# Kernel tuning notes

Measured on AMD Instinct MI355X. Metric: run time of the kernel, lower is better.

Reference implementation:

```python
import jax, jax.numpy as jnp
import numpy as np

N = 2_000_000   # points
B = 4           # batch
C = 32          # feature channels
H = 512         # image height (== round(K[0,0]))
W = 512         # image width
GRID = 64       # grid_resolution


def setup_inputs() -> dict:
    key = jax.random.key(0)
    k1, k2, k3 = jax.random.split(key, 3)
    bids = jax.random.randint(k1, (N, 1), 0, B)
    coords = jax.random.randint(k2, (N, 3), 0, GRID)
    dense_coords = jnp.concatenate([bids, coords], axis=1).astype(jnp.int32)  # [N,4]
    pixel_features = jax.random.normal(k3, (B, C, H, W), dtype=jnp.float32)
    K = jnp.array([[512.0, 0.0, 256.0],
                   [0.0, 512.0, 256.0],
                   [0.0, 0.0, 1.0]], dtype=jnp.float32)
    P = jnp.array([[1.0, 0.0, 0.0, 0.0],
                   [0.0, 1.0, 0.0, 0.0],
                   [0.0, 0.0, 1.0, 3.0],
                   [0.0, 0.0, 0.0, 1.0]], dtype=jnp.float32)
    return {"dense_coords": dense_coords, "pixel_features": pixel_features, "K": K, "P": P}


def reference(dense_coords, pixel_features, K, P):
    grid_res = GRID
    batch_ids = dense_coords[:, 0]
    grid_pos = dense_coords[:, 1:].astype(pixel_features.dtype)
    # grid coords -> world positions in [-1, 1]
    world = grid_pos * (2.0 / (grid_res - 1)) - 1.0  # [N,3]
    ones = jnp.ones((world.shape[0], 1), world.dtype)
    pts_h = jnp.concatenate([world, ones], axis=1)   # [N,4]
    # project: camera = P @ pts^T, normalize by homogeneous coord
    cam = pts_h @ P.T                                # [N,4]
    cam = cam / cam[:, 3:4]
    img_h = cam[:, :3] @ K.T                         # [N,3]
    img_h = img_h / img_h[:, 2:3]
    image_x = img_h[:, 0]   # js (columns)
    image_y = img_h[:, 1]   # is (rows)
    points_depth = cam[:, 2:3]                       # [N,1]

    i0f = jnp.floor(image_y)
    j0f = jnp.floor(image_x)
    di = (image_y - i0f)[:, None]                    # [N,1]
    dj = (image_x - j0f)[:, None]                    # [N,1]

    Hh = pixel_features.shape[2]
    Ww = pixel_features.shape[3]
    i0 = jnp.clip(i0f.astype(jnp.int32), 0, Hh - 1)
    i1 = jnp.clip(i0f.astype(jnp.int32) + 1, 0, Hh - 1)
    j0 = jnp.clip(j0f.astype(jnp.int32), 0, Ww - 1)
    j1 = jnp.clip(j0f.astype(jnp.int32) + 1, 0, Ww - 1)

    b = batch_ids
    # four gathers, each [N, C] (advanced indices split by ':' -> result dims first)
    f00 = pixel_features[b, :, i0, j0]
    f10 = pixel_features[b, :, i1, j0]
    f01 = pixel_features[b, :, i0, j1]
    f11 = pixel_features[b, :, i1, j1]

    mean_j = (1.0 - di) * f00 + di * f10
    mean_jp = (1.0 - di) * f01 + di * f11
    feature_bilinear = (1.0 - dj) * mean_j + dj * mean_jp  # [N,C]
    return feature_bilinear, points_depth
```

## Files before the change

### kernel.cpp

```cpp
#include <hip/hip_runtime.h>

#define GRID_RES 64
#define C_CH     32
#define H_IMG    512
#define W_IMG    512

typedef float    f32x4 __attribute__((ext_vector_type(4)));
typedef int      i32x4 __attribute__((ext_vector_type(4)));
typedef unsigned u32x4 __attribute__((ext_vector_type(4)));

__device__ __forceinline__ ushort f32_to_bf16(float f) {
    union { float f; unsigned u; } a; a.f = f;
    unsigned r = (a.u + 0x7FFFu + ((a.u >> 16) & 1u)) >> 16;
    return (ushort)r;
}
__device__ __forceinline__ float bf16lo_to_f32(unsigned u) {
    union { unsigned u; float f; } a; a.u = u << 16; return a.f;
}
__device__ __forceinline__ float bf16hi_to_f32(unsigned u) {
    union { unsigned u; float f; } a; a.u = u & 0xFFFF0000u; return a.f;
}

__global__ __launch_bounds__(256) void transpose_bf16_kernel(
    const float* __restrict__ in, ushort* __restrict__ out)
{
    const int HW = H_IMG * W_IMG;
    __shared__ float tile[C_CH * 65];

    const int tilesPerBatch = HW / 64;
    const int b   = blockIdx.x / tilesPerBatch;
    const int t   = blockIdx.x % tilesPerBatch;
    const int hw0 = t * 64;
    const int tid = threadIdx.x;

    const int c_r = tid >> 3;
    const int u_r = (tid & 7) * 8;
    const f32x4* src = (const f32x4*)(in + ((size_t)(b * C_CH + c_r) * HW + hw0 + u_r));
    f32x4 v0 = __builtin_nontemporal_load(src);
    f32x4 v1 = __builtin_nontemporal_load(src + 1);
    float* d = &tile[c_r * 65 + u_r];
    d[0] = v0.x; d[1] = v0.y; d[2] = v0.z; d[3] = v0.w;
    d[4] = v1.x; d[5] = v1.y; d[6] = v1.z; d[7] = v1.w;

    __syncthreads();

    const int u_w = tid >> 2;
    const int c0  = (tid & 3) * 8;
    union { ushort us[8]; uint4 v; } pk;
#pragma unroll
    for (int k = 0; k < 8; ++k)
        pk.us[k] = f32_to_bf16(tile[(c0 + k) * 65 + u_w]);
    *(uint4*)(out + ((size_t)(b * HW + hw0 + u_w) * C_CH + c0)) = pk.v;
}

__global__ __launch_bounds__(256) void gather_bf16_kernel(
    const int*    __restrict__ coords,
    const ushort* __restrict__ feat,
    const float*  __restrict__ Km,
    const float*  __restrict__ Pm,
    float* __restrict__ out_feat,
    float* __restrict__ out_depth,
    int N)
{
    __shared__ int   s_base[256];
    __shared__ int   s_dji[256];
    __shared__ int   s_dii[256];
    __shared__ float s_fdi[256];
    __shared__ float s_fdj[256];

    const int tid = threadIdx.x;
    const int p0  = blockIdx.x * 256;

    {
        const int p = p0 + tid;
        if (p < N) {
            i32x4 cc = __builtin_nontemporal_load((const i32x4*)coords + p);
            const float s = 2.0f / (float)(GRID_RES - 1);
            float wx = (float)cc.y * s - 1.0f;
            float wy = (float)cc.z * s - 1.0f;
            float wz = (float)cc.w * s - 1.0f;

            float cam0 = Pm[0]  * wx + Pm[1]  * wy + Pm[2]  * wz + Pm[3];
            float cam1 = Pm[4]  * wx + Pm[5]  * wy + Pm[6]  * wz + Pm[7];
            float cam2 = Pm[8]  * wx + Pm[9]  * wy + Pm[10] * wz + Pm[11];
            float cam3 = Pm[12] * wx + Pm[13] * wy + Pm[14] * wz + Pm[15];
            cam0 /= cam3; cam1 /= cam3; cam2 /= cam3;

            float g0 = Km[0] * cam0 + Km[1] * cam1 + Km[2] * cam2;
            float g1 = Km[3] * cam0 + Km[4] * cam1 + Km[5] * cam2;
            float g2 = Km[6] * cam0 + Km[7] * cam1 + Km[8] * cam2;
            float image_x = g0 / g2;
            float image_y = g1 / g2;

            float i0f = floorf(image_y);
            float j0f = floorf(image_x);
            float di = image_y - i0f;
            float dj = image_x - j0f;
            i0f = fminf(fmaxf(i0f, -1.0e9f), 1.0e9f);
            j0f = fminf(fmaxf(j0f, -1.0e9f), 1.0e9f);
            int i0r = (int)i0f;
            int j0r = (int)j0f;
            int i0 = min(max(i0r,     0), H_IMG - 1);
            int i1 = min(max(i0r + 1, 0), H_IMG - 1);
            int j0 = min(max(j0r,     0), W_IMG - 1);
            int j1 = min(max(j0r + 1, 0), W_IMG - 1);
            int b  = cc.x;

            s_base[tid] = ((b * H_IMG + i0) * W_IMG + j0) * C_CH;
            s_dji[tid]  = (j1 - j0) * C_CH;
            s_dii[tid]  = (i1 - i0) * W_IMG * C_CH;
            s_fdi[tid]  = di;
            s_fdj[tid]  = dj;
            __builtin_nontemporal_store(cam2, out_depth + p);
        }
    }
    __syncthreads();

    const int cq   = tid & 3;
    const int slot = tid >> 2;
#pragma unroll
    for (int it = 0; it < 4; ++it) {
        const int lp = it * 64 + slot;
        const int p  = p0 + lp;
        if (p < N) {
            const int   base = s_base[lp] + cq * 8;
            const int   dji  = s_dji[lp];
            const int   dii  = s_dii[lp];
            const float fdi  = s_fdi[lp];
            const float fdj  = s_fdj[lp];

            const u32x4 u00 = *(const u32x4*)(feat + base);
            const u32x4 u01 = *(const u32x4*)(feat + base + dji);
            const u32x4 u10 = *(const u32x4*)(feat + base + dii);
            const u32x4 u11 = *(const u32x4*)(feat + base + dii + dji);

            float o[8];
            const unsigned* a00 = (const unsigned*)&u00;
            const unsigned* a01 = (const unsigned*)&u01;
            const unsigned* a10 = (const unsigned*)&u10;
            const unsigned* a11 = (const unsigned*)&u11;
#pragma unroll
            for (int k = 0; k < 4; ++k) {
                float f00 = bf16lo_to_f32(a00[k]), f01 = bf16lo_to_f32(a01[k]);
                float f10 = bf16lo_to_f32(a10[k]), f11 = bf16lo_to_f32(a11[k]);
                float r0 = f00 + fdi * (f10 - f00);
                float r1 = f01 + fdi * (f11 - f01);
                o[2 * k] = r0 + fdj * (r1 - r0);
                f00 = bf16hi_to_f32(a00[k]); f01 = bf16hi_to_f32(a01[k]);
                f10 = bf16hi_to_f32(a10[k]); f11 = bf16hi_to_f32(a11[k]);
                r0 = f00 + fdi * (f10 - f00);
                r1 = f01 + fdi * (f11 - f01);
                o[2 * k + 1] = r0 + fdj * (r1 - r0);
            }
            float* op = out_feat + (size_t)p * C_CH + cq * 8;
            f32x4 lo4 = { o[0], o[1], o[2], o[3] };
            f32x4 hi4 = { o[4], o[5], o[6], o[7] };
            __builtin_nontemporal_store(lo4, (f32x4*)op);
            __builtin_nontemporal_store(hi4, (f32x4*)(op + 4));
        }
    }
}

__global__ __launch_bounds__(256) void gather_fp32_direct_kernel(
    const int*   __restrict__ coords,
    const float* __restrict__ feat,
    const float* __restrict__ Km,
    const float* __restrict__ Pm,
    float* __restrict__ out_feat,
    float* __restrict__ out_depth,
    int N)
{
    __shared__ int   s_base[64];
    __shared__ int   s_dji[64];
    __shared__ int   s_dii[64];
    __shared__ float s_fdi[64];
    __shared__ float s_fdj[64];

    const int tid = threadIdx.x;
    const int p0  = blockIdx.x * 64;
    const int HW  = H_IMG * W_IMG;

    if (tid < 64) {
        const int p = p0 + tid;
        if (p < N) {
            int4 cc = ((const int4*)coords)[p];
            const float s = 2.0f / (float)(GRID_RES - 1);
            float wx = (float)cc.y * s - 1.0f;
            float wy = (float)cc.z * s - 1.0f;
            float wz = (float)cc.w * s - 1.0f;
            float cam0 = Pm[0]  * wx + Pm[1]  * wy + Pm[2]  * wz + Pm[3];
            float cam1 = Pm[4]  * wx + Pm[5]  * wy + Pm[6]  * wz + Pm[7];
            float cam2 = Pm[8]  * wx + Pm[9]  * wy + Pm[10] * wz + Pm[11];
            float cam3 = Pm[12] * wx + Pm[13] * wy + Pm[14] * wz + Pm[15];
            cam0 /= cam3; cam1 /= cam3; cam2 /= cam3;
            float g0 = Km[0] * cam0 + Km[1] * cam1 + Km[2] * cam2;
            float g1 = Km[3] * cam0 + Km[4] * cam1 + Km[5] * cam2;
            float g2 = Km[6] * cam0 + Km[7] * cam1 + Km[8] * cam2;
            float image_x = g0 / g2;
            float image_y = g1 / g2;
            float i0f = floorf(image_y);
            float j0f = floorf(image_x);
            float di = image_y - i0f;
            float dj = image_x - j0f;
            i0f = fminf(fmaxf(i0f, -1.0e9f), 1.0e9f);
            j0f = fminf(fmaxf(j0f, -1.0e9f), 1.0e9f);
            int i0r = (int)i0f;
            int j0r = (int)j0f;
            int i0 = min(max(i0r,     0), H_IMG - 1);
            int i1 = min(max(i0r + 1, 0), H_IMG - 1);
            int j0 = min(max(j0r,     0), W_IMG - 1);
            int j1 = min(max(j0r + 1, 0), W_IMG - 1);
            int b  = cc.x;
            s_base[tid] = (b * C_CH * H_IMG + i0) * W_IMG + j0;
            s_dji[tid]  = (j1 - j0);
            s_dii[tid]  = (i1 - i0) * W_IMG;
            s_fdi[tid]  = di;
            s_fdj[tid]  = dj;
            out_depth[p] = cam2;
        }
    }
    __syncthreads();

    const int c      = tid & 31;
    const int lpBase = tid >> 5;
#pragma unroll
    for (int it = 0; it < 8; ++it) {
        const int lp = it * 8 + lpBase;
        const int p  = p0 + lp;
        if (p < N) {
            const int   base = s_base[lp];
            const int   dji  = s_dji[lp];
            const int   dii  = s_dii[lp];
            const float fdi  = s_fdi[lp];
            const float fdj  = s_fdj[lp];
            const float* fp = feat + base + (size_t)c * HW;
            float f00 = fp[0];
            float f01 = fp[dji];
            float f10 = fp[dii];
            float f11 = fp[dii + dji];
            float r0 = f00 + fdi * (f10 - f00);
            float r1 = f01 + fdi * (f11 - f01);
            out_feat[(size_t)p * C_CH + c] = r0 + fdj * (r1 - r0);
        }
    }
}

extern "C" void kernel_launch(void* const* d_in, const int* in_sizes, int n_in,
                              void* d_out, int out_size, void* d_ws, size_t ws_size,
                              hipStream_t stream)
{
    const int*   coords = (const int*)  d_in[0];
    const float* feat   = (const float*)d_in[1];
    const float* Km     = (const float*)d_in[2];
    const float* Pm     = (const float*)d_in[3];

    const int N  = in_sizes[0] / 4;
    const int Bb = in_sizes[1] / (C_CH * H_IMG * W_IMG);
    const int HW = H_IMG * W_IMG;

    float* out_feat  = (float*)d_out;
    float* out_depth = out_feat + (size_t)N * C_CH;

    const size_t need = (size_t)in_sizes[1] * sizeof(ushort);

    if (ws_size >= need) {
        ushort* tfeat = (ushort*)d_ws;
        transpose_bf16_kernel<<<Bb * (HW / 64), 256, 0, stream>>>(feat, tfeat);
        const int nblocks = (N + 255) / 256;
        gather_bf16_kernel<<<nblocks, 256, 0, stream>>>(
            coords, tfeat, Km, Pm, out_feat, out_depth, N);
    } else {
        const int nblocks = (N + 63) / 64;
        gather_fp32_direct_kernel<<<nblocks, 64, 0, stream>>>(
            coords, feat, Km, Pm, out_feat, out_depth, N);
    }
}
```

Baseline: 474.7 us.

## Bin points by image tile via counting sort before bf16 bilinear gather

```diff
diff --git a/kernel.cpp b/kernel.cpp
--- a/kernel.cpp
+++ b/kernel.cpp
@@ -4,6 +4,7 @@
 #define C_CH     32
 #define H_IMG    512
 #define W_IMG    512
+#define NBINS    512
 
 typedef float    f32x4 __attribute__((ext_vector_type(4)));
 typedef int      i32x4 __attribute__((ext_vector_type(4)));
@@ -19,6 +20,58 @@
 }
 __device__ __forceinline__ float bf16hi_to_f32(unsigned u) {
     union { unsigned u; float f; } a; a.u = u & 0xFFFF0000u; return a.f;
+}
+
+struct ProjOut {
+    int   base;
+    int   dji;
+    int   dii;
+    float di, dj, depth;
+    int   bin;
+};
+__device__ __forceinline__ ProjOut project_pt(
+    const i32x4 cc, const float* __restrict__ Km, const float* __restrict__ Pm)
+{
+    const float s = 2.0f / (float)(GRID_RES - 1);
+    float wx = (float)cc.y * s - 1.0f;
+    float wy = (float)cc.z * s - 1.0f;
+    float wz = (float)cc.w * s - 1.0f;
+
+    float cam0 = Pm[0]  * wx + Pm[1]  * wy + Pm[2]  * wz + Pm[3];
+    float cam1 = Pm[4]  * wx + Pm[5]  * wy + Pm[6]  * wz + Pm[7];
+    float cam2 = Pm[8]  * wx + Pm[9]  * wy + Pm[10] * wz + Pm[11];
+    float cam3 = Pm[12] * wx + Pm[13] * wy + Pm[14] * wz + Pm[15];
+    cam0 /= cam3; cam1 /= cam3; cam2 /= cam3;
+
+    float g0 = Km[0] * cam0 + Km[1] * cam1 + Km[2] * cam2;
+    float g1 = Km[3] * cam0 + Km[4] * cam1 + Km[5] * cam2;
+    float g2 = Km[6] * cam0 + Km[7] * cam1 + Km[8] * cam2;
+    float image_x = g0 / g2;
+    float image_y = g1 / g2;
+
+    float i0f = floorf(image_y);
+    float j0f = floorf(image_x);
+    float di = image_y - i0f;
+    float dj = image_x - j0f;
+    i0f = fminf(fmaxf(i0f, -1.0e9f), 1.0e9f);
+    j0f = fminf(fmaxf(j0f, -1.0e9f), 1.0e9f);
+    int i0r = (int)i0f;
+    int j0r = (int)j0f;
+    int i0 = min(max(i0r,     0), H_IMG - 1);
+    int i1 = min(max(i0r + 1, 0), H_IMG - 1);
+    int j0 = min(max(j0r,     0), W_IMG - 1);
+    int j1 = min(max(j0r + 1, 0), W_IMG - 1);
+    int b  = cc.x;
+
+    ProjOut o;
+    o.base  = ((b * H_IMG + i0) * W_IMG + j0) * C_CH;
+    o.dji   = (j1 - j0) * C_CH;
+    o.dii   = (i1 - i0) * W_IMG * C_CH;
+    o.di    = di;
+    o.dj    = dj;
+    o.depth = cam2;
+    o.bin   = b * 128 + (i0 >> 5) * 8 + (j0 >> 6);
+    return o;
 }
 
 __global__ __launch_bounds__(256) void transpose_bf16_kernel(
@@ -53,6 +106,180 @@
     *(uint4*)(out + ((size_t)(b * HW + hw0 + u_w) * C_CH + c0)) = pk.v;
 }
 
+__global__ __launch_bounds__(512) void init_hist_kernel(int* __restrict__ hist)
+{
+    hist[threadIdx.x] = 0;
+}
+
+__global__ __launch_bounds__(256) void hist_kernel(
+    const int* __restrict__ coords,
+    const float* __restrict__ Km, const float* __restrict__ Pm,
+    int* __restrict__ hist, int N)
+{
+    __shared__ int lh[NBINS];
+    const int tid = threadIdx.x;
+    for (int i = tid; i < NBINS; i += 256) lh[i] = 0;
+    __syncthreads();
+
+    for (int p = blockIdx.x * 256 + tid; p < N; p += gridDim.x * 256) {
+        i32x4 cc = __builtin_nontemporal_load((const i32x4*)coords + p);
+        ProjOut o = project_pt(cc, Km, Pm);
+        atomicAdd(&lh[o.bin], 1);
+    }
+    __syncthreads();
+    for (int i = tid; i < NBINS; i += 256)
+        if (lh[i]) atomicAdd(&hist[i], lh[i]);
+}
+
+__global__ __launch_bounds__(512) void scan_kernel(
+    const int* __restrict__ hist, int* __restrict__ cursor)
+{
+    __shared__ int tmp[NBINS];
+    const int t = threadIdx.x;
+    const int v = hist[t];
+    tmp[t] = v;
+    __syncthreads();
+    for (int off = 1; off < NBINS; off <<= 1) {
+        int a = (t >= off) ? tmp[t - off] : 0;
+        __syncthreads();
+        tmp[t] += a;
+        __syncthreads();
+    }
+    cursor[t] = tmp[t] - v;
+}
+
+__global__ __launch_bounds__(1024) void scatter_kernel(
+    const int* __restrict__ coords,
+    const float* __restrict__ Km, const float* __restrict__ Pm,
+    int* __restrict__ cursor,
+    i32x4* __restrict__ records,
+    float* __restrict__ out_depth, int N)
+{
+    __shared__ int lh[NBINS];
+    __shared__ int lbase[NBINS];
+    const int tid = threadIdx.x;
+    const int p0  = blockIdx.x * 4096;
+
+    for (int i = tid; i < NBINS; i += 1024) lh[i] = 0;
+    __syncthreads();
+
+    int      binA[4], rankA[4], baseA[4];
+    unsigned pfA[4];
+    float    diA[4], djA[4];
+#pragma unroll
+    for (int k = 0; k < 4; ++k) {
+        const int pp = p0 + k * 1024 + tid;
+        binA[k] = -1;
+        if (pp < N) {
+            i32x4 cc = __builtin_nontemporal_load((const i32x4*)coords + pp);
+            ProjOut o = project_pt(cc, Km, Pm);
+            binA[k]  = o.bin;
+            baseA[k] = o.base;
+            diA[k]   = o.di;
+            djA[k]   = o.dj;
+            pfA[k]   = (unsigned)pp
+                     | ((unsigned)(o.dji != 0) << 30)
+                     | ((unsigned)(o.dii != 0) << 31);
+            rankA[k] = atomicAdd(&lh[o.bin], 1);
+            __builtin_nontemporal_store(o.depth, out_depth + pp);
+        }
+    }
+    __syncthreads();
+
+    for (int i = tid; i < NBINS; i += 1024) {
+        int c = lh[i];
+        if (c) lbase[i] = atomicAdd(&cursor[i], c);
+    }
+    __syncthreads();
+
+#pragma unroll
+    for (int k = 0; k < 4; ++k) {
+        if (binA[k] >= 0) {
+            const int slot = lbase[binA[k]] + rankA[k];
+            i32x4 rec;
+            rec.x = baseA[k];
+            rec.y = (int)pfA[k];
+            rec.z = __float_as_int(diA[k]);
+            rec.w = __float_as_int(djA[k]);
+            records[slot] = rec;
+        }
+    }
+}
+
+__global__ __launch_bounds__(256) void gather_sorted_kernel(
+    const i32x4*  __restrict__ records,
+    const ushort* __restrict__ feat,
+    float* __restrict__ out_feat,
+    int N, int swz_q, int swz_r)
+{
+    const int orig = blockIdx.x;
+    const int xcd  = orig & 7;
+    const int idx  = orig >> 3;
+    const int wg   = (xcd < swz_r ? xcd * (swz_q + 1)
+                                  : swz_r * (swz_q + 1) + (xcd - swz_r) * swz_q) + idx;
+    const int s0   = wg * 256;
+
+    __shared__ int   s_base[256];
+    __shared__ unsigned s_pf[256];
+    __shared__ float s_di[256];
+    __shared__ float s_dj[256];
+
+    const int tid = threadIdx.x;
+    if (s0 + tid < N) {
+        i32x4 rec = __builtin_nontemporal_load(records + s0 + tid);
+        s_base[tid] = rec.x;
+        s_pf[tid]   = (unsigned)rec.y;
+        s_di[tid]   = __int_as_float(rec.z);
+        s_dj[tid]   = __int_as_float(rec.w);
+    }
+    __syncthreads();
+
+    const int cq   = tid & 3;
+    const int slot = tid >> 2;
+#pragma unroll
+    for (int it = 0; it < 4; ++it) {
+        const int lp = it * 64 + slot;
+        if (s0 + lp < N) {
+            const unsigned pf  = s_pf[lp];
+            const int   base = s_base[lp] + cq * 8;
+            const int   dji  = (int)((pf >> 30) & 1u) << 5;
+            const int   dii  = (int)((pf >> 31) & 1u) << 14;
+            const int   pidx = (int)(pf & 0x3FFFFFFFu);
+            const float fdi  = s_di[lp];
+            const float fdj  = s_dj[lp];
+
+            const u32x4 u00 = *(const u32x4*)(feat + base);
+            const u32x4 u01 = *(const u32x4*)(feat + base + dji);
+            const u32x4 u10 = *(const u32x4*)(feat + base + dii);
+            const u32x4 u11 = *(const u32x4*)(feat + base + dii + dji);
+
+            float o[8];
+            const unsigned* a00 = (const unsigned*)&u00;
+            const unsigned* a01 = (const unsigned*)&u01;
+            const unsigned* a10 = (const unsigned*)&u10;
+            const unsigned* a11 = (const unsigned*)&u11;
+#pragma unroll
+            for (int k = 0; k < 4; ++k) {
+                float f00 = bf16lo_to_f32(a00[k]), f01 = bf16lo_to_f32(a01[k]);
+                float f10 = bf16lo_to_f32(a10[k]), f11 = bf16lo_to_f32(a11[k]);
+                float r0 = f00 + fdi * (f10 - f00);
+                float r1 = f01 + fdi * (f11 - f01);
+                o[2 * k] = r0 + fdj * (r1 - r0);
+                f00 = bf16hi_to_f32(a00[k]); f01 = bf16hi_to_f32(a01[k]);
+                f10 = bf16hi_to_f32(a10[k]); f11 = bf16hi_to_f32(a11[k]);
+                r0 = f00 + fdi * (f10 - f00);
+                r1 = f01 + fdi * (f11 - f01);
+                o[2 * k + 1] = r0 + fdj * (r1 - r0);
+            }
+            float* op = out_feat + (size_t)pidx * C_CH + cq * 8;
+            f32x4 lo4 = { o[0], o[1], o[2], o[3] };
+            f32x4 hi4 = { o[4], o[5], o[6], o[7] };
+            __builtin_nontemporal_store(lo4, (f32x4*)op);
+            __builtin_nontemporal_store(hi4, (f32x4*)(op + 4));
+        }
+    }
+}
+
 __global__ __launch_bounds__(256) void gather_bf16_kernel(
     const int*    __restrict__ coords,
     const ushort* __restrict__ feat,
@@ -75,43 +302,13 @@
         const int p = p0 + tid;
         if (p < N) {
             i32x4 cc = __builtin_nontemporal_load((const i32x4*)coords + p);
-            const float s = 2.0f / (float)(GRID_RES - 1);
-            float wx = (float)cc.y * s - 1.0f;
-            float wy = (float)cc.z * s - 1.0f;
-            float wz = (float)cc.w * s - 1.0f;
-
-            float cam0 = Pm[0]  * wx + Pm[1]  * wy + Pm[2]  * wz + Pm[3];
-            float cam1 = Pm[4]  * wx + Pm[5]  * wy + Pm[6]  * wz + Pm[7];
-            float cam2 = Pm[8]  * wx + Pm[9]  * wy + Pm[10] * wz + Pm[11];
-            float cam3 = Pm[12] * wx + Pm[13] * wy + Pm[14] * wz + Pm[15];
-            cam0 /= cam3; cam1 /= cam3; cam2 /= cam3;
-
-            float g0 = Km[0] * cam0 + Km[1] * cam1 + Km[2] * cam2;
-            float g1 = Km[3] * cam0 + Km[4] * cam1 + Km[5] * cam2;
-            float g2 = Km[6] * cam0 + Km[7] * cam1 + Km[8] * cam2;
-            float image_x = g0 / g2;
-            float image_y = g1 / g2;
-
-            float i0f = floorf(image_y);
-            float j0f = floorf(image_x);
-            float di = image_y - i0f;
-            float dj = image_x - j0f;
-            i0f = fminf(fmaxf(i0f, -1.0e9f), 1.0e9f);
-            j0f = fminf(fmaxf(j0f, -1.0e9f), 1.0e9f);
-            int i0r = (int)i0f;
-            int j0r = (int)j0f;
-            int i0 = min(max(i0r,     0), H_IMG - 1);
-            int i1 = min(max(i0r + 1, 0), H_IMG - 1);
-            int j0 = min(max(j0r,     0), W_IMG - 1);
-            int j1 = min(max(j0r + 1, 0), W_IMG - 1);
-            int b  = cc.x;
-
-            s_base[tid] = ((b * H_IMG + i0) * W_IMG + j0) * C_CH;
-            s_dji[tid]  = (j1 - j0) * C_CH;
-            s_dii[tid]  = (i1 - i0) * W_IMG * C_CH;
-            s_fdi[tid]  = di;
-            s_fdj[tid]  = dj;
-            __builtin_nontemporal_store(cam2, out_depth + p);
+            ProjOut o = project_pt(cc, Km, Pm);
+            s_base[tid] = o.base;
+            s_dji[tid]  = o.dji;
+            s_dii[tid]  = o.dii;
+            s_fdi[tid]  = o.di;
+            s_fdj[tid]  = o.dj;
+            __builtin_nontemporal_store(o.depth, out_depth + p);
         }
     }
     __syncthreads();
@@ -161,7 +358,7 @@
     }
 }
 
-__global__ __launch_bounds__(256) void gather_fp32_direct_kernel(
+__global__ __launch_bounds__(64) void gather_fp32_direct_kernel(
     const int*   __restrict__ coords,
     const float* __restrict__ feat,
     const float* __restrict__ Km,
@@ -170,20 +367,20 @@
     float* __restrict__ out_depth,
     int N)
 {
-    __shared__ int   s_base[64];
-    __shared__ int   s_dji[64];
-    __shared__ int   s_dii[64];
-    __shared__ float s_fdi[64];
-    __shared__ float s_fdj[64];
-
-    const int tid = threadIdx.x;
-    const int p0  = blockIdx.x * 64;
+    const int tid = threadIdx.x;
+    const int p0  = blockIdx.x * 2;
     const int HW  = H_IMG * W_IMG;
 
-    if (tid < 64) {
+    __shared__ int   s_base[2];
+    __shared__ int   s_dji[2];
+    __shared__ int   s_dii[2];
+    __shared__ float s_fdi[2];
+    __shared__ float s_fdj[2];
+
+    if (tid < 2) {
         const int p = p0 + tid;
         if (p < N) {
-            int4 cc = ((const int4*)coords)[p];
+            i32x4 cc = ((const i32x4*)coords)[p];
             const float s = 2.0f / (float)(GRID_RES - 1);
             float wx = (float)cc.y * s - 1.0f;
             float wy = (float)cc.z * s - 1.0f;
@@ -221,27 +418,23 @@
     }
     __syncthreads();
 
-    const int c      = tid & 31;
-    const int lpBase = tid >> 5;
-#pragma unroll
-    for (int it = 0; it < 8; ++it) {
-        const int lp = it * 8 + lpBase;
-        const int p  = p0 + lp;
-        if (p < N) {
-            const int   base = s_base[lp];
-            const int   dji  = s_dji[lp];
-            const int   dii  = s_dii[lp];
-            const float fdi  = s_fdi[lp];
-            const float fdj  = s_fdj[lp];
-            const float* fp = feat + base + (size_t)c * HW;
-            float f00 = fp[0];
-            float f01 = fp[dji];
-            float f10 = fp[dii];
-            float f11 = fp[dii + dji];
-            float r0 = f00 + fdi * (f10 - f00);
-            float r1 = f01 + fdi * (f11 - f01);
-            out_feat[(size_t)p * C_CH + c] = r0 + fdj * (r1 - r0);
-        }
+    const int c  = tid & 31;
+    const int lp = tid >> 5;
+    const int p  = p0 + lp;
+    if (p < N) {
+        const int   base = s_base[lp];
+        const int   dji  = s_dji[lp];
+        const int   dii  = s_dii[lp];
+        const float fdi  = s_fdi[lp];
+        const float fdj  = s_fdj[lp];
+        const float* fp = feat + base + (size_t)c * HW;
+        float f00 = fp[0];
+        float f01 = fp[dji];
+        float f10 = fp[dii];
+        float f11 = fp[dii + dji];
+        float r0 = f00 + fdi * (f10 - f00);
+        float r1 = f01 + fdi * (f11 - f01);
+        out_feat[(size_t)p * C_CH + c] = r0 + fdj * (r1 - r0);
     }
 }
 
@@ -255,23 +448,43 @@
     const float* Pm     = (const float*)d_in[3];
 
     const int N  = in_sizes[0] / 4;
-    const int Bb = in_sizes[1] / (C_CH * H_IMG * W_IMG);
     const int HW = H_IMG * W_IMG;
+    const int Bb = in_sizes[1] / (C_CH * HW);
 
     float* out_feat  = (float*)d_out;
     float* out_depth = out_feat + (size_t)N * C_CH;
 
-    const size_t need = (size_t)in_sizes[1] * sizeof(ushort);
-
-    if (ws_size >= need) {
+    const size_t map_bytes  = (size_t)in_sizes[1] * sizeof(ushort);
+    const size_t rec_bytes  = (size_t)N * 16;
+    const size_t hist_bytes = NBINS * sizeof(int);
+    const size_t need_full  = map_bytes + rec_bytes + 2 * hist_bytes + 256;
+
+    if (ws_size >= need_full) {
+        char* ws = (char*)d_ws;
+        ushort* tfeat   = (ushort*)ws;                      ws += map_bytes;
+        i32x4*  records = (i32x4*)ws;                       ws += rec_bytes;
+        int*    hist    = (int*)ws;                         ws += hist_bytes;
+        int*    cursor  = (int*)ws;
+
+        const int nwg = (N + 255) / 256;
+        const int swz_q = nwg / 8;
+        const int swz_r = nwg % 8;
+
+        transpose_bf16_kernel<<<Bb * (HW / 64), 256, 0, stream>>>(feat, tfeat);
+        init_hist_kernel<<<1, NBINS, 0, stream>>>(hist);
+        hist_kernel<<<2048, 256, 0, stream>>>(coords, Km, Pm, hist, N);
+        scan_kernel<<<1, NBINS, 0, stream>>>(hist, cursor);
+        scatter_kernel<<<(N + 4095) / 4096, 1024, 0, stream>>>(
+            coords, Km, Pm, cursor, records, out_depth, N);
+        gather_sorted_kernel<<<nwg, 256, 0, stream>>>(
+            records, tfeat, out_feat, N, swz_q, swz_r);
+    } else if (ws_size >= map_bytes) {
         ushort* tfeat = (ushort*)d_ws;
         transpose_bf16_kernel<<<Bb * (HW / 64), 256, 0, stream>>>(feat, tfeat);
-        const int nblocks = (N + 255) / 256;
-        gather_bf16_kernel<<<nblocks, 256, 0, stream>>>(
+        gather_bf16_kernel<<<(N + 255) / 256, 256, 0, stream>>>(
             coords, tfeat, Km, Pm, out_feat, out_depth, N);
     } else {
-        const int nblocks = (N + 63) / 64;
-        gather_fp32_direct_kernel<<<nblocks, 64, 0, stream>>>(
+        gather_fp32_direct_kernel<<<(N + 1) / 2, 64, 0, stream>>>(
             coords, feat, Km, Pm, out_feat, out_depth, N);
     }
 }
```

After: 475.2 us. About the same (+0.1%).
